# Optimization experiments

Hardware: AMD Instinct MI355X
Metric: run time of the kernel (lower is better)

Reference implementation:

```python
import jax, jax.numpy as jnp
import numpy as np

D_MODEL = 768; D_STATE = 64; D_CONV = 7; EXPAND = 2; HEADDIM = 64; NGROUPS = 1; CHUNK = 256
D_INNER = EXPAND * D_MODEL                                      # 1536
NHEADS = D_INNER // HEADDIM                                     # 24
D_IN_PROJ = 2 * D_INNER + 2 * NGROUPS * D_STATE + 2 * NHEADS    # 3248
CONV_DIM = D_INNER + 2 * NGROUPS * D_STATE                      # 1664
BATCH, SEQLEN = 2, 4096
EPS = 1e-5


def setup_inputs() -> dict:
    key = jax.random.key(0)
    ks = jax.random.split(key, 8)
    w = lambda k, shape, s=0.02: jax.random.normal(k, shape, jnp.float32) * s
    # dt in [1e-3, 1e-1], dt_bias = softplus^{-1}(dt)
    dt0 = jnp.exp(jax.random.uniform(ks[3], (NHEADS,)) * (np.log(0.1) - np.log(0.001)) + np.log(0.001))
    return {
        "x": jax.random.normal(ks[0], (BATCH, SEQLEN, D_MODEL), jnp.float32),
        "ln_w": jnp.ones((D_MODEL,), jnp.float32),
        "ln_b": jnp.zeros((D_MODEL,), jnp.float32),
        "in_proj_w": w(ks[1], (D_IN_PROJ, D_MODEL)),
        "conv_w": w(ks[2], (CONV_DIM, D_CONV), 0.2),
        "conv_b": jnp.zeros((CONV_DIM,), jnp.float32),
        "dt_bias": dt0 + jnp.log(-jnp.expm1(-dt0)),
        "A_log": jnp.log(jax.random.uniform(ks[4], (NHEADS,), minval=1.0, maxval=16.0)),
        "D": jnp.ones((NHEADS,), jnp.float32),
        "fc_D_w": w(ks[5], (NHEADS, D_INNER)),
        "rms_w": jnp.ones((D_INNER,), jnp.float32),
        "out_proj_w": w(ks[6], (D_MODEL, D_INNER)),
    }


def _segsum(a):
    # a: (..., T) -> (..., T, T) lower-triangular segment sums, -inf above diagonal
    T = a.shape[-1]
    cs = jnp.cumsum(a, -1)
    ss = cs[..., :, None] - cs[..., None, :]
    return jnp.where(jnp.tril(jnp.ones((T, T), bool)), ss, -jnp.inf)


def _ssd(X, A, Bm, Cm):
    # Chunked SSD scan (mamba_chunk_scan_combined, D=None, z=None, ngroups=1).
    # X: (b,l,h,p) already scaled by dt; A: (b,l,h) = dt*A_head; Bm,Cm: (b,l,n)
    b, l, h, p = X.shape
    c = l // CHUNK
    X = X.reshape(b, c, CHUNK, h, p)
    A = A.reshape(b, c, CHUNK, h).transpose(0, 3, 1, 2)  # (b,h,c,l)
    Bm = Bm.reshape(b, c, CHUNK, D_STATE)
    Cm = Cm.reshape(b, c, CHUNK, D_STATE)
    A_cum = jnp.cumsum(A, -1)
    Lmat = jnp.exp(_segsum(A))                                      # (b,h,c,l,s)
    Y_diag = jnp.einsum("bcln,bcsn,bhcls,bcshp->bclhp", Cm, Bm, Lmat, X)
    decay_states = jnp.exp(A_cum[..., -1:] - A_cum)                 # (b,h,c,l)
    states = jnp.einsum("bcln,bhcl,bclhp->bchpn", Bm, decay_states, X)
    A_chunk = jnp.pad(A_cum[..., -1], ((0, 0), (0, 0), (1, 0)))     # (b,h,c+1)
    decay_chunk = jnp.exp(_segsum(A_chunk))                         # (b,h,c+1,c+1)
    all_states = jnp.concatenate([jnp.zeros_like(states[:, :1]), states], 1)
    prev = jnp.einsum("bhzc,bchpn->bzhpn", decay_chunk, all_states)[:, :-1]
    Y_off = jnp.einsum("bcln,bchpn,bhcl->bclhp", Cm, prev, jnp.exp(A_cum))
    return (Y_diag + Y_off).reshape(b, l, h, p)


def _dwconv_causal(x, w, b):
    # x: (B,L,C), w: (C,K); torch Conv1d(padding=K-1) then [:, :L] == causal conv
    xp = jnp.pad(x, ((0, 0), (D_CONV - 1, 0), (0, 0))).transpose(0, 2, 1)
    y = jax.lax.conv_general_dilated(xp, w[:, None, :], (1,), "VALID",
                                     feature_group_count=CONV_DIM,
                                     dimension_numbers=("NCH", "OIH", "NCH"))
    return y.transpose(0, 2, 1) + b


def _forward(x, ln_w, ln_b, in_proj_w, conv_w, conv_b, dt_bias, A_log, D, fc_D_w, rms_w, out_proj_w):
    B, L, _ = x.shape
    # pre-LayerNorm
    mu = jnp.mean(x, -1, keepdims=True)
    var = jnp.mean((x - mu) ** 2, -1, keepdims=True)
    u = (x - mu) * jax.lax.rsqrt(var + EPS) * ln_w + ln_b
    # input projection -> z | xBC | dt_fw,dt_bw
    zxbcdt = u @ in_proj_w.T
    z = zxbcdt[..., :D_INNER]
    xBC = zxbcdt[..., D_INNER:D_INNER + CONV_DIM]
    dt2 = zxbcdt[..., -2 * NHEADS:]
    dt = jnp.concatenate([dt2[..., :NHEADS], jnp.flip(dt2[..., NHEADS:], 1)], 0)  # (2B,L,H)
    dt = jax.nn.softplus(dt + dt_bias)
    A = -jnp.exp(A_log)
    # causal depthwise conv + SiLU
    xBC = jax.nn.silu(_dwconv_causal(xBC, conv_w, conv_b))
    xs = xBC[..., :D_INNER]
    Bm = xBC[..., D_INNER:D_INNER + D_STATE]
    Cm = xBC[..., D_INNER + D_STATE:]
    x_og = xs
    cat2 = lambda t: jnp.concatenate([t, jnp.flip(t, 1)], 0)  # fwd + reversed copy
    X = cat2(xs).reshape(2 * B, L, NHEADS, HEADDIM) * dt[..., None]
    y = _ssd(X, dt * A, cat2(Bm), cat2(Cm)).reshape(2 * B, L, D_INNER)
    # quasiseparable combine: shift each direction by one, zero the boundary
    y = jnp.roll(y, 1, axis=1).at[:, 0, :].set(0.0)
    y = y[:B] + jnp.flip(y[B:], 1)
    # data-dependent diagonal term
    Dterm = x_og @ fc_D_w.T + D                                 # (B,L,H)
    y = y + x_og * jnp.repeat(Dterm, HEADDIM, axis=-1)
    # gated RMSNorm
    y = y * jax.nn.silu(z)
    y = y * jax.lax.rsqrt(jnp.mean(y * y, -1, keepdims=True) + EPS) * rms_w
    # out projection + residual (dropout=0 -> identity)
    return y @ out_proj_w.T + x


def reference(x, ln_w, ln_b, in_proj_w, conv_w, conv_b, dt_bias, A_log, D, fc_D_w, rms_w, out_proj_w):
    return _forward(x, ln_w, ln_b, in_proj_w, conv_w, conv_b, dt_bias, A_log, D, fc_D_w, rms_w, out_proj_w)
```

## Files before the change

### kernel.cpp

```cpp
#include <hip/hip_runtime.h>
#include <hip/hip_bf16.h>
#include <cstdint>
#include <cstddef>

typedef __hip_bfloat16 bf16;
typedef __attribute__((ext_vector_type(8))) short short8;
typedef __attribute__((ext_vector_type(4))) float f32x4;

#define B_   2
#define L_   4096
#define DM_  768
#define DI_  1536
#define NH_  24
#define HD_  64
#define DS_  64
#define CH_  256
#define NC_  16
#define CD_  1664
#define DIP_ 3248
#define EPS_ 1e-5f

#define ROWS_ (B_*L_)
#define BB4_  (2*B_)

#define LDSK 40
#define LDT  72

__device__ __forceinline__ float b2f(bf16 v) { return __bfloat162float(v); }
__device__ __forceinline__ bf16  f2b(float v) { return __float2bfloat16(v); }
__device__ __forceinline__ float sb2f(short s) {
    bf16 t; __builtin_memcpy(&t, &s, 2); return __bfloat162float(t);
}
__device__ __forceinline__ short f2s(float v) {
    bf16 t = __float2bfloat16(v); short s; __builtin_memcpy(&s, &t, 2); return s;
}

__global__ __launch_bounds__(256) void cast_f2b(const float* __restrict__ s,
                                                bf16* __restrict__ d, int n) {
    int i = (blockIdx.x * 256 + threadIdx.x) * 4;
    if (i + 3 < n) {
        float4 v = *(const float4*)(s + i);
        d[i]   = f2b(v.x); d[i+1] = f2b(v.y);
        d[i+2] = f2b(v.z); d[i+3] = f2b(v.w);
    } else {
        for (int k = i; k < n; k++) d[k] = f2b(s[k]);
    }
}

__global__ __launch_bounds__(256) void ln_kernel(const float* __restrict__ x,
                                                 const float* __restrict__ w,
                                                 const float* __restrict__ bb,
                                                 bf16* __restrict__ u) {
    int row = blockIdx.x, tid = threadIdx.x;
    const float* xr = x + (size_t)row * DM_;
    float v0 = xr[tid], v1 = xr[tid + 256], v2 = xr[tid + 512];
    float s = v0 + v1 + v2;
    float q = v0*v0 + v1*v1 + v2*v2;
    for (int off = 32; off > 0; off >>= 1) {
        s += __shfl_down(s, off);
        q += __shfl_down(q, off);
    }
    __shared__ float rs[4], rq[4];
    __shared__ float mean_s, rstd_s;
    int lane = tid & 63, wid = tid >> 6;
    if (!lane) { rs[wid] = s; rq[wid] = q; }
    __syncthreads();
    if (!tid) {
        float S = rs[0]+rs[1]+rs[2]+rs[3];
        float Q = rq[0]+rq[1]+rq[2]+rq[3];
        float mu = S / (float)DM_;
        float var = Q / (float)DM_ - mu*mu;
        mean_s = mu; rstd_s = rsqrtf(var + EPS_);
    }
    __syncthreads();
    float mu = mean_s, rstd = rstd_s;
    bf16* ur = u + (size_t)row * DM_;
    ur[tid]       = f2b((v0 - mu) * rstd * w[tid]       + bb[tid]);
    ur[tid + 256] = f2b((v1 - mu) * rstd * w[tid + 256] + bb[tid + 256]);
    ur[tid + 512] = f2b((v2 - mu) * rstd * w[tid + 512] + bb[tid + 512]);
}

__global__ __launch_bounds__(256) void gemm_bf16_inproj(const bf16* __restrict__ A,
                                                        const bf16* __restrict__ W,
                                                        bf16* __restrict__ zbuf,
                                                        bf16* __restrict__ xbc,
                                                        float* __restrict__ dtr) {
    __shared__ short As[128 * LDSK];
    __shared__ short Ws[128 * LDSK];
    int tid = threadIdx.x;
    int wave = tid >> 6, lane = tid & 63;
    int wm = (wave >> 1) * 64, wn = (wave & 1) * 64;
    int bm = blockIdx.y * 128, bn = blockIdx.x * 128;
    f32x4 acc[4][4] = {};
    int lr = tid >> 1;
    int lseg = (tid & 1) * 16;
    const int K = DM_;
    int fr = lane & 15, kg = (lane >> 4) * 8;
    for (int k0 = 0; k0 < K; k0 += 32) {
        const short* ag = (const short*)A + (size_t)(bm + lr) * K + k0 + lseg;
        short8 av0 = *(const short8*)ag;
        short8 av1 = *(const short8*)(ag + 8);
        short8 wv0 = {}, wv1 = {};
        int n = bn + lr;
        if (n < DIP_) {
            const short* wg = (const short*)W + (size_t)n * K + k0 + lseg;
            wv0 = *(const short8*)wg;
            wv1 = *(const short8*)(wg + 8);
        }
        __syncthreads();
        *(short8*)&As[lr*LDSK + lseg]     = av0;
        *(short8*)&As[lr*LDSK + lseg + 8] = av1;
        *(short8*)&Ws[lr*LDSK + lseg]     = wv0;
        *(short8*)&Ws[lr*LDSK + lseg + 8] = wv1;
        __syncthreads();
        short8 af[4], wf[4];
        #pragma unroll
        for (int i = 0; i < 4; i++)
            af[i] = *(const short8*)&As[(wm + i*16 + fr)*LDSK + kg];
        #pragma unroll
        for (int j = 0; j < 4; j++)
            wf[j] = *(const short8*)&Ws[(wn + j*16 + fr)*LDSK + kg];
        #pragma unroll
        for (int i = 0; i < 4; i++)
            #pragma unroll
            for (int j = 0; j < 4; j++)
                acc[i][j] = __builtin_amdgcn_mfma_f32_16x16x32_bf16(af[i], wf[j], acc[i][j], 0, 0, 0);
    }
    int rg = (lane >> 4) * 4;
    #pragma unroll
    for (int i = 0; i < 4; i++) {
        int mrow = bm + wm + i*16 + rg;
        #pragma unroll
        for (int j = 0; j < 4; j++) {
            int ncol = bn + wn + j*16 + fr;
            #pragma unroll
            for (int r = 0; r < 4; r++) {
                float v = acc[i][j][r];
                int m = mrow + r;
                if (ncol < DI_)            zbuf[(size_t)m * DI_ + ncol] = f2b(v);
                else if (ncol < DI_ + CD_) xbc[(size_t)m * CD_ + (ncol - DI_)] = f2b(v);
                else if (ncol < DIP_)      dtr[(size_t)m * 48 + (ncol - DI_ - CD_)] = v;
            }
        }
    }
}

__global__ __launch_bounds__(256) void gemm_bf16_out(const bf16* __restrict__ A,
                                                     const bf16* __restrict__ W,
                                                     const float* __restrict__ resid,
                                                     float* __restrict__ C) {
    __shared__ short As[128 * LDSK];
    __shared__ short Ws[128 * LDSK];
    int tid = threadIdx.x;
    int wave = tid >> 6, lane = tid & 63;
    int wm = (wave >> 1) * 64, wn = (wave & 1) * 64;
    int bm = blockIdx.y * 128, bn = blockIdx.x * 128;
    f32x4 acc[4][4] = {};
    int lr = tid >> 1;
    int lseg = (tid & 1) * 16;
    const int K = DI_;
    int fr = lane & 15, kg = (lane >> 4) * 8;
    for (int k0 = 0; k0 < K; k0 += 32) {
        const short* ag = (const short*)A + (size_t)(bm + lr) * K + k0 + lseg;
        short8 av0 = *(const short8*)ag;
        short8 av1 = *(const short8*)(ag + 8);
        const short* wg = (const short*)W + (size_t)(bn + lr) * K + k0 + lseg;
        short8 wv0 = *(const short8*)wg;
        short8 wv1 = *(const short8*)(wg + 8);
        __syncthreads();
        *(short8*)&As[lr*LDSK + lseg]     = av0;
        *(short8*)&As[lr*LDSK + lseg + 8] = av1;
        *(short8*)&Ws[lr*LDSK + lseg]     = wv0;
        *(short8*)&Ws[lr*LDSK + lseg + 8] = wv1;
        __syncthreads();
        short8 af[4], wf[4];
        #pragma unroll
        for (int i = 0; i < 4; i++)
            af[i] = *(const short8*)&As[(wm + i*16 + fr)*LDSK + kg];
        #pragma unroll
        for (int j = 0; j < 4; j++)
            wf[j] = *(const short8*)&Ws[(wn + j*16 + fr)*LDSK + kg];
        #pragma unroll
        for (int i = 0; i < 4; i++)
            #pragma unroll
            for (int j = 0; j < 4; j++)
                acc[i][j] = __builtin_amdgcn_mfma_f32_16x16x32_bf16(af[i], wf[j], acc[i][j], 0, 0, 0);
    }
    int rg = (lane >> 4) * 4;
    #pragma unroll
    for (int i = 0; i < 4; i++) {
        int mrow = bm + wm + i*16 + rg;
        #pragma unroll
        for (int j = 0; j < 4; j++) {
            int ncol = bn + wn + j*16 + fr;
            #pragma unroll
            for (int r = 0; r < 4; r++) {
                int m = mrow + r;
                C[(size_t)m * DM_ + ncol] = acc[i][j][r] + resid[(size_t)m * DM_ + ncol];
            }
        }
    }
}

__global__ __launch_bounds__(256) void conv_kernel(const bf16* __restrict__ xbc,
                                                   const float* __restrict__ cw,
                                                   const float* __restrict__ cb,
                                                   bf16* __restrict__ out) {
    size_t idx = (size_t)blockIdx.x * 256 + threadIdx.x;
    if (idx >= (size_t)ROWS_ * CD_) return;
    int c = idx % CD_;
    int t = (idx / CD_) % L_;
    int b = idx / ((size_t)CD_ * L_);
    float acc = cb[c];
    #pragma unroll
    for (int j = 0; j < 7; j++) {
        int tt = t - 6 + j;
        if (tt >= 0)
            acc += b2f(xbc[((size_t)(b * L_ + tt)) * CD_ + c]) * cw[c * 7 + j];
    }
    acc = acc / (1.f + __expf(-acc));
    out[idx] = f2b(acc);
}

__global__ __launch_bounds__(256) void dt_kernel(const float* __restrict__ dtr,
                                                 const float* __restrict__ dt_bias,
                                                 float* __restrict__ dt4) {
    int idx = blockIdx.x * 256 + threadIdx.x;
    if (idx >= BB4_ * L_ * NH_) return;
    int h = idx % NH_;
    int t = (idx / NH_) % L_;
    int bbx = idx / (NH_ * L_);
    int bp = bbx & 1;
    float raw;
    if (bbx < 2) raw = dtr[((size_t)(bp * L_ + t)) * 48 + h];
    else         raw = dtr[((size_t)(bp * L_ + (L_ - 1 - t))) * 48 + NH_ + h];
    float v = raw + dt_bias[h];
    float dt = (v > 20.f) ? v : log1pf(__expf(v));
    dt4[idx] = dt;
}

__global__ __launch_bounds__(256) void scan_kernel(const float* __restrict__ dt4,
                                                   const float* __restrict__ A_log,
                                                   float* __restrict__ Acum) {
    int bid = blockIdx.x;
    int c  = bid % NC_;
    int h  = (bid / NC_) % NH_;
    int bbx = bid / (NC_ * NH_);
    int l = threadIdx.x;
    float Ah = -__expf(A_log[h]);
    float val = dt4[((size_t)(bbx * L_) + c * CH_ + l) * NH_ + h] * Ah;
    __shared__ float sc[256];
    sc[l] = val; __syncthreads();
    for (int off = 1; off < 256; off <<= 1) {
        float t = (l >= off) ? sc[l - off] : 0.f;
        __syncthreads();
        sc[l] += t;
        __syncthreads();
    }
    Acum[(size_t)bid * CH_ + l] = sc[l];
}

__global__ __launch_bounds__(256) void states_kernel(const bf16* __restrict__ conv,
                                                     const float* __restrict__ dt4,
                                                     const float* __restrict__ Acum,
                                                     bf16* __restrict__ states) {
    int bid = blockIdx.x;
    int h = bid % NH_;
    int c = (bid / NH_) % NC_;
    int bbx = bid / (NH_ * NC_);
    int bp = bbx & 1;
    bool flip = bbx >= 2;
    int tid = threadIdx.x;
    int wave = tid >> 6, lane = tid & 63;
    int wr = wave >> 1, wc = wave & 1;
    int fr = lane & 15, kg = (lane >> 4) * 8, rg = (lane >> 4) * 4;
    size_t abase = ((size_t)(bbx * NH_ + h) * NC_ + c) * CH_;
    float Atot = Acum[abase + CH_ - 1];

    __shared__ short Xt[64 * LDT];
    __shared__ short Bdt[64 * LDT];
    f32x4 acc[2][2] = {};

    for (int lt = 0; lt < 4; lt++) {
        __syncthreads();
        int l = tid & 63;
        int q0 = (tid >> 6) * 8;
        int t = c * CH_ + lt * 64 + l;
        int tt = flip ? (L_ - 1 - t) : t;
        const short* crow = (const short*)conv + (size_t)(bp * L_ + tt) * CD_;
        float dtv = dt4[((size_t)(bbx * L_) + t) * NH_ + h];
        float decay = __expf(Atot - Acum[abase + lt * 64 + l]);
        #pragma unroll
        for (int half = 0; half < 2; half++) {
            int qq = q0 + half * 32;
            short8 xv = *(const short8*)(crow + h * HD_ + qq);
            short8 bv = *(const short8*)(crow + DI_ + qq);
            #pragma unroll
            for (int k = 0; k < 8; k++) {
                Xt[(qq + k) * LDT + l]  = f2s(sb2f(xv[k]) * dtv);
                Bdt[(qq + k) * LDT + l] = f2s(sb2f(bv[k]) * decay);
            }
        }
        __syncthreads();
        #pragma unroll
        for (int ks = 0; ks < 2; ks++) {
            short8 af[2], wf[2];
            #pragma unroll
            for (int i = 0; i < 2; i++)
                af[i] = *(const short8*)&Xt[(wr*32 + i*16 + fr)*LDT + ks*32 + kg];
            #pragma unroll
            for (int j = 0; j < 2; j++)
                wf[j] = *(const short8*)&Bdt[(wc*32 + j*16 + fr)*LDT + ks*32 + kg];
            #pragma unroll
            for (int i = 0; i < 2; i++)
                #pragma unroll
                for (int j = 0; j < 2; j++)
                    acc[i][j] = __builtin_amdgcn_mfma_f32_16x16x32_bf16(af[i], wf[j], acc[i][j], 0, 0, 0);
        }
    }
    size_t sbase = (size_t)bid * 4096;
    #pragma unroll
    for (int i = 0; i < 2; i++)
        #pragma unroll
        for (int j = 0; j < 2; j++)
            #pragma unroll
            for (int r = 0; r < 4; r++) {
                int p = wr*32 + i*16 + rg + r;
                int n = wc*32 + j*16 + fr;
                states[sbase + p*64 + n] = f2b(acc[i][j][r]);
            }
}

__global__ __launch_bounds__(256) void chunkscan_kernel(const bf16* __restrict__ states,
                                                        const float* __restrict__ Acum,
                                                        bf16* __restrict__ prev) {
    int bid = blockIdx.x;
    int h = bid % NH_;
    int bbx = bid / NH_;
    int tid = threadIdx.x;
    float run[16];
    #pragma unroll
    for (int k = 0; k < 16; k++) run[k] = 0.f;
    for (int c = 0; c < NC_; c++) {
        float Tc = Acum[((size_t)(bbx * NH_ + h) * NC_ + c) * CH_ + CH_ - 1];
        float ec = __expf(Tc);
        size_t base = ((size_t)(bbx * NC_ + c) * NH_ + h) * 4096;
        #pragma unroll
        for (int k = 0; k < 16; k++) {
            size_t e = tid + k * 256;
            prev[base + e] = f2b(run[k]);
            run[k] = run[k] * ec + b2f(states[base + e]);
        }
    }
}

__global__ __launch_bounds__(256) void ydiag_kernel(const bf16* __restrict__ conv,
                                                    const float* __restrict__ dt4,
                                                    const float* __restrict__ Acum,
                                                    const bf16* __restrict__ prev,
                                                    bf16* __restrict__ yc,
                                                    int pass) {
    int bid = blockIdx.x;
    int lt = bid & 3;
    int q  = bid >> 2;
    int h  = q % NH_;
    int r2 = q / NH_;
    int c  = r2 % NC_;
    int b  = r2 / NC_;
    int bbx = pass ? (b + 2) : b;
    int bp = b;
    bool flip = pass != 0;
    int tid = threadIdx.x;
    int wave = tid >> 6, lane = tid & 63;
    int wr = wave >> 1, wc = wave & 1;
    int fr = lane & 15, kg = (lane >> 4) * 8, rg = (lane >> 4) * 4;
    size_t abase = ((size_t)(bbx * NH_ + h) * NC_ + c) * CH_;

    __shared__ short Ct[64 * LDT];
    __shared__ short Pt[64 * LDT];
    __shared__ short Xt[64 * LDT];
    __shared__ short Gt[64 * LDT];
    __shared__ float aL[64], aS[64];

    #pragma unroll
    for (int it = 0; it < 2; it++) {
        int li = tid + it * 256;
        int l = li >> 3, cs = (li & 7) * 8;
        int t = c * CH_ + lt * 64 + l;
        int tt = flip ? (L_ - 1 - t) : t;
        *(short8*)&Ct[l * LDT + cs] =
            *(const short8*)((const short*)conv + (size_t)(bp * L_ + tt) * CD_ + DI_ + DS_ + cs);
    }
    {
        size_t pbase = ((size_t)(bbx * NC_ + c) * NH_ + h) * 4096;
        #pragma unroll
        for (int it = 0; it < 2; it++) {
            int li = tid + it * 256;
            int p = li >> 3, cs = (li & 7) * 8;
            *(short8*)&Pt[p * LDT + cs] =
                *(const short8*)((const short*)prev + pbase + p * 64 + cs);
        }
    }
    if (tid < 64) aL[tid] = Acum[abase + lt * 64 + tid];
    __syncthreads();

    f32x4 acc[2][2] = {};
    #pragma unroll
    for (int ks = 0; ks < 2; ks++) {
        short8 af[2], wf[2];
        #pragma unroll
        for (int i = 0; i < 2; i++)
            af[i] = *(const short8*)&Ct[(wr*32 + i*16 + fr)*LDT + ks*32 + kg];
        #pragma unroll
        for (int j = 0; j < 2; j++)
            wf[j] = *(const short8*)&Pt[(wc*32 + j*16 + fr)*LDT + ks*32 + kg];
        #pragma unroll
        for (int i = 0; i < 2; i++)
            #pragma unroll
            for (int j = 0; j < 2; j++)
                acc[i][j] = __builtin_amdgcn_mfma_f32_16x16x32_bf16(af[i], wf[j], acc[i][j], 0, 0, 0);
    }
    #pragma unroll
    for (int i = 0; i < 2; i++)
        #pragma unroll
        for (int r = 0; r < 4; r++) {
            float e = __expf(aL[wr*32 + i*16 + rg + r]);
            #pragma unroll
            for (int j = 0; j < 2; j++) acc[i][j][r] *= e;
        }

    for (int st = 0; st <= lt; st++) {
        __syncthreads();
        #pragma unroll
        for (int it = 0; it < 2; it++) {
            int li = tid + it * 256;
            int s = li >> 3, cs = (li & 7) * 8;
            int t = c * CH_ + st * 64 + s;
            int tt = flip ? (L_ - 1 - t) : t;
            *(short8*)&Pt[s * LDT + cs] =
                *(const short8*)((const short*)conv + (size_t)(bp * L_ + tt) * CD_ + DI_ + cs);
        }
        {
            int s = tid & 63;
            int p0 = (tid >> 6) * 8;
            int t = c * CH_ + st * 64 + s;
            int tt = flip ? (L_ - 1 - t) : t;
            const short* crow = (const short*)conv + (size_t)(bp * L_ + tt) * CD_ + h * HD_;
            float dtv = dt4[((size_t)(bbx * L_) + t) * NH_ + h];
            #pragma unroll
            for (int half = 0; half < 2; half++) {
                int p = p0 + half * 32;
                short8 xv = *(const short8*)(crow + p);
                #pragma unroll
                for (int k = 0; k < 8; k++)
                    Xt[(p + k) * LDT + s] = f2s(sb2f(xv[k]) * dtv);
            }
        }
        if (tid < 64) aS[tid] = Acum[abase + st * 64 + tid];
        __syncthreads();
        f32x4 gacc[2][2] = {};
        #pragma unroll
        for (int ks = 0; ks < 2; ks++) {
            short8 af[2], wf[2];
            #pragma unroll
            for (int i = 0; i < 2; i++)
                af[i] = *(const short8*)&Ct[(wr*32 + i*16 + fr)*LDT + ks*32 + kg];
            #pragma unroll
            for (int j = 0; j < 2; j++)
                wf[j] = *(const short8*)&Pt[(wc*32 + j*16 + fr)*LDT + ks*32 + kg];
            #pragma unroll
            for (int i = 0; i < 2; i++)
                #pragma unroll
                for (int j = 0; j < 2; j++)
                    gacc[i][j] = __builtin_amdgcn_mfma_f32_16x16x32_bf16(af[i], wf[j], gacc[i][j], 0, 0, 0);
        }
        #pragma unroll
        for (int i = 0; i < 2; i++)
            #pragma unroll
            for (int j = 0; j < 2; j++)
                #pragma unroll
                for (int r = 0; r < 4; r++) {
                    int ll = wr*32 + i*16 + rg + r;
                    int ss = wc*32 + j*16 + fr;
                    bool valid = (st < lt) || (ll >= ss);
                    float g = valid ? gacc[i][j][r] * __expf(aL[ll] - aS[ss]) : 0.f;
                    Gt[ll * LDT + ss] = f2s(g);
                }
        __syncthreads();
        #pragma unroll
        for (int ks = 0; ks < 2; ks++) {
            short8 af[2], wf[2];
            #pragma unroll
            for (int i = 0; i < 2; i++)
                af[i] = *(const short8*)&Gt[(wr*32 + i*16 + fr)*LDT + ks*32 + kg];
            #pragma unroll
            for (int j = 0; j < 2; j++)
                wf[j] = *(const short8*)&Xt[(wc*32 + j*16 + fr)*LDT + ks*32 + kg];
            #pragma unroll
            for (int i = 0; i < 2; i++)
                #pragma unroll
                for (int j = 0; j < 2; j++)
                    acc[i][j] = __builtin_amdgcn_mfma_f32_16x16x32_bf16(af[i], wf[j], acc[i][j], 0, 0, 0);
        }
    }

    #pragma unroll
    for (int i = 0; i < 2; i++)
        #pragma unroll
        for (int r = 0; r < 4; r++) {
            int l = wr*32 + i*16 + rg + r;
            int t = c * CH_ + lt * 64 + l;
            #pragma unroll
            for (int j = 0; j < 2; j++) {
                int p = wc*32 + j*16 + fr;
                float v = acc[i][j][r];
                if (!pass) {
                    int pos = t + 1;
                    if (pos == L_)
                        yc[((size_t)(b * L_)) * DI_ + h * HD_ + p] = f2b(0.f);
                    else
                        yc[((size_t)(b * L_) + pos) * DI_ + h * HD_ + p] = f2b(v);
                } else {
                    int pos = L_ - 2 - t;
                    if (pos >= 0) {
                        size_t o = ((size_t)(b * L_) + pos) * DI_ + h * HD_ + p;
                        yc[o] = f2b(b2f(yc[o]) + v);
                    }
                }
            }
        }
}

__global__ __launch_bounds__(256) void combine_kernel(const bf16* __restrict__ yc,
                                                      const bf16* __restrict__ conv,
                                                      const bf16* __restrict__ zbuf,
                                                      const float* __restrict__ fcD,
                                                      const float* __restrict__ Dvec,
                                                      const float* __restrict__ rms_w,
                                                      bf16* __restrict__ ybuf) {
    int row = blockIdx.x;
    int tid = threadIdx.x;
    __shared__ float xog_s[DI_];
    __shared__ float dterm_s[NH_];
    __shared__ float rs[4];
    __shared__ float scale_s;
    float yv[6], xog[6], zv[6];
    const bf16* convrow = conv + (size_t)row * CD_;
    const bf16* zrow = zbuf + (size_t)row * DI_;
    const bf16* ycrow = yc + (size_t)row * DI_;
    #pragma unroll
    for (int k = 0; k < 6; k++) {
        int d = tid + k * 256;
        float xo = b2f(convrow[d]);
        xog[k] = xo; xog_s[d] = xo;
        zv[k] = b2f(zrow[d]);
        yv[k] = b2f(ycrow[d]);
    }
    __syncthreads();
    int wid = tid >> 6, lane = tid & 63;
    for (int hh = 0; hh < 6; hh++) {
        int h = wid * 6 + hh;
        float s = 0.f;
        #pragma unroll
        for (int k = 0; k < 24; k++) {
            int d = lane + k * 64;
            s += xog_s[d] * fcD[(size_t)h * DI_ + d];
        }
        for (int off = 32; off > 0; off >>= 1) s += __shfl_down(s, off);
        if (!lane) dterm_s[h] = s + Dvec[h];
    }
    __syncthreads();
    float ss = 0.f;
    #pragma unroll
    for (int k = 0; k < 6; k++) {
        int d = tid + k * 256;
        int h = d >> 6;
        float y = yv[k] + xog[k] * dterm_s[h];
        float z = zv[k];
        y *= z / (1.f + __expf(-z));
        yv[k] = y;
        ss += y * y;
    }
    for (int off = 32; off > 0; off >>= 1) ss += __shfl_down(ss, off);
    if (!lane) rs[wid] = ss;
    __syncthreads();
    if (!tid) scale_s = rsqrtf((rs[0]+rs[1]+rs[2]+rs[3]) / (float)DI_ + EPS_);
    __syncthreads();
    float sc = scale_s;
    bf16* yrow = ybuf + (size_t)row * DI_;
    #pragma unroll
    for (int k = 0; k < 6; k++) {
        int d = tid + k * 256;
        yrow[d] = f2b(yv[k] * sc * rms_w[d]);
    }
}

extern "C" void kernel_launch(void* const* d_in, const int* in_sizes, int n_in,
                              void* d_out, int out_size, void* d_ws, size_t ws_size,
                              hipStream_t stream) {
    const float* x        = (const float*)d_in[0];
    const float* ln_w     = (const float*)d_in[1];
    const float* ln_b     = (const float*)d_in[2];
    const float* in_proj  = (const float*)d_in[3];
    const float* conv_w   = (const float*)d_in[4];
    const float* conv_b   = (const float*)d_in[5];
    const float* dt_bias  = (const float*)d_in[6];
    const float* A_log    = (const float*)d_in[7];
    const float* Dvec     = (const float*)d_in[8];
    const float* fc_D_w   = (const float*)d_in[9];
    const float* rms_w    = (const float*)d_in[10];
    const float* out_proj = (const float*)d_in[11];
    float* out = (float*)d_out;

    uint8_t* base = (uint8_t*)d_ws;
    size_t off = 0;
    auto alloc = [&](size_t bytes) -> void* {
        void* p = base + off;
        off += (bytes + 255) & ~(size_t)255;
        return p;
    };
    bf16*  buf_z    = (bf16*) alloc((size_t)ROWS_ * DI_ * 2);
    uint8_t* regA   = (uint8_t*)alloc((size_t)ROWS_ * CD_ * 2);
    float* buf_dtr  = (float*)alloc((size_t)ROWS_ * 48 * 4);
    bf16*  buf_conv = (bf16*) alloc((size_t)ROWS_ * CD_ * 2);
    float* buf_dt   = (float*)alloc((size_t)BB4_ * L_ * NH_ * 4);
    float* buf_acum = (float*)alloc((size_t)BB4_ * NH_ * NC_ * CH_ * 4);
    uint8_t* regB   = (uint8_t*)alloc((size_t)ROWS_ * DM_ * 4);
    bf16*  w_in_bf  = (bf16*) alloc((size_t)DIP_ * DM_ * 2);
    bf16*  w_out_bf = (bf16*) alloc((size_t)DM_ * DI_ * 2);

    bf16*  buf_xbc  = (bf16*)regA;
    bf16*  buf_st   = (bf16*)regA;
    bf16*  buf_prev = buf_st + (size_t)BB4_ * NC_ * NH_ * 4096;
    bf16*  buf_y    = (bf16*)regA;
    bf16*  buf_u    = (bf16*)regB;
    bf16*  buf_yc   = (bf16*)regB;

    cast_f2b<<<(DIP_ * DM_ / 4 + 255) / 256, 256, 0, stream>>>(in_proj, w_in_bf, DIP_ * DM_);
    cast_f2b<<<(DM_ * DI_ / 4 + 255) / 256, 256, 0, stream>>>(out_proj, w_out_bf, DM_ * DI_);
    ln_kernel<<<ROWS_, 256, 0, stream>>>(x, ln_w, ln_b, buf_u);
    gemm_bf16_inproj<<<dim3((DIP_ + 127) / 128, ROWS_ / 128), 256, 0, stream>>>(
        buf_u, w_in_bf, buf_z, buf_xbc, buf_dtr);
    {
        size_t tot = (size_t)ROWS_ * CD_;
        conv_kernel<<<(tot + 255) / 256, 256, 0, stream>>>(buf_xbc, conv_w, conv_b, buf_conv);
    }
    dt_kernel<<<(BB4_ * L_ * NH_) / 256, 256, 0, stream>>>(buf_dtr, dt_bias, buf_dt);
    scan_kernel<<<BB4_ * NH_ * NC_, 256, 0, stream>>>(buf_dt, A_log, buf_acum);
    states_kernel<<<BB4_ * NC_ * NH_, 256, 0, stream>>>(buf_conv, buf_dt, buf_acum, buf_st);
    chunkscan_kernel<<<BB4_ * NH_, 256, 0, stream>>>(buf_st, buf_acum, buf_prev);
    ydiag_kernel<<<B_ * NC_ * NH_ * 4, 256, 0, stream>>>(buf_conv, buf_dt, buf_acum, buf_prev, buf_yc, 0);
    ydiag_kernel<<<B_ * NC_ * NH_ * 4, 256, 0, stream>>>(buf_conv, buf_dt, buf_acum, buf_prev, buf_yc, 1);
    combine_kernel<<<ROWS_, 256, 0, stream>>>(buf_yc, buf_conv, buf_z, fc_D_w, Dvec, rms_w, buf_y);
    gemm_bf16_out<<<dim3(DM_ / 128, ROWS_ / 128), 256, 0, stream>>>(
        buf_y, w_out_bf, x, out);
}
```

Measured before the change: 547.6 us.

## Pretranspose dt-scaled X and B, vectorize conv, load MFMA operands from global

Adds an xt_kernel that writes dt-scaled X and raw B once into time-contiguous transposed buffers. The states and ydiag kernels then read their MFMA fragments directly from global memory instead of rebuilding LDS tiles with scalar transposes in every block and every inner step. The depthwise conv is rewritten so each thread handles 8 channels by 4 timesteps with vector loads and reused weights, and chunkscan now works in place on a single states buffer. The cost is an extra kernel, two new workspace buffers and more global traffic for the transposed copies.

```diff
diff --git a/kernel.cpp b/kernel.cpp
--- a/kernel.cpp
+++ b/kernel.cpp
@@ -206,20 +206,55 @@
                                                    const float* __restrict__ cw,
                                                    const float* __restrict__ cb,
                                                    bf16* __restrict__ out) {
-    size_t idx = (size_t)blockIdx.x * 256 + threadIdx.x;
-    if (idx >= (size_t)ROWS_ * CD_) return;
-    int c = idx % CD_;
-    int t = (idx / CD_) % L_;
-    int b = idx / ((size_t)CD_ * L_);
-    float acc = cb[c];
-    #pragma unroll
-    for (int j = 0; j < 7; j++) {
-        int tt = t - 6 + j;
-        if (tt >= 0)
-            acc += b2f(xbc[((size_t)(b * L_ + tt)) * CD_ + c]) * cw[c * 7 + j];
-    }
-    acc = acc / (1.f + __expf(-acc));
-    out[idx] = f2b(acc);
+    int g = blockIdx.x * 256 + threadIdx.x;
+    int cg = g % 208;
+    int tq = g / 208;
+    int b = tq >> 10;
+    int t0 = (tq & 1023) * 4;
+    int c8 = cg * 8;
+    const short* src = (const short*)xbc + (size_t)(b * L_) * CD_ + c8;
+
+    float w[7][8], acc[4][8];
+    #pragma unroll
+    for (int k = 0; k < 8; k++) {
+        #pragma unroll
+        for (int j = 0; j < 7; j++) w[j][k] = cw[(c8 + k) * 7 + j];
+        float bias = cb[c8 + k];
+        #pragma unroll
+        for (int q = 0; q < 4; q++) acc[q][k] = bias;
+    }
+    #pragma unroll
+    for (int m = 0; m < 10; m++) {
+        int tt = t0 - 6 + m;
+        float row[8];
+        if (tt >= 0) {
+            short8 v = *(const short8*)(src + (size_t)tt * CD_);
+            #pragma unroll
+            for (int k = 0; k < 8; k++) row[k] = sb2f(v[k]);
+        } else {
+            #pragma unroll
+            for (int k = 0; k < 8; k++) row[k] = 0.f;
+        }
+        #pragma unroll
+        for (int q = 0; q < 4; q++) {
+            int j = m - q;
+            if (j >= 0 && j < 7) {
+                #pragma unroll
+                for (int k = 0; k < 8; k++) acc[q][k] += row[k] * w[j][k];
+            }
+        }
+    }
+    #pragma unroll
+    for (int q = 0; q < 4; q++) {
+        short8 o;
+        #pragma unroll
+        for (int k = 0; k < 8; k++) {
+            float a = acc[q][k];
+            a = a / (1.f + __expf(-a));
+            o[k] = f2s(a);
+        }
+        *(short8*)((short*)out + (size_t)(b * L_ + t0 + q) * CD_ + c8) = o;
+    }
 }
 
 __global__ __launch_bounds__(256) void dt_kernel(const float* __restrict__ dtr,
@@ -260,57 +295,91 @@
     Acum[(size_t)bid * CH_ + l] = sc[l];
 }
 
-__global__ __launch_bounds__(256) void states_kernel(const bf16* __restrict__ conv,
-                                                     const float* __restrict__ dt4,
+__global__ __launch_bounds__(256) void xt_kernel(const bf16* __restrict__ conv,
+                                                 const float* __restrict__ dt4,
+                                                 bf16* __restrict__ XT,
+                                                 bf16* __restrict__ BT) {
+    int bid = blockIdx.x;
+    int hh = bid % 25;
+    int c  = (bid / 25) % NC_;
+    int bbx = bid / (25 * NC_);
+    int bp = bbx & 1;
+    bool flip = bbx >= 2;
+    bool isB = (hh == NH_);
+    int coff = isB ? DI_ : hh * HD_;
+    int tid = threadIdx.x;
+    __shared__ short tile[64][72];
+    short* dstb = (short*)(isB ? BT : XT);
+    size_t rowbase = isB ? (size_t)(bbx * 64) : (size_t)((bbx * NH_ + hh) * 64);
+    for (int lt = 0; lt < 4; lt++) {
+        __syncthreads();
+        #pragma unroll
+        for (int it = 0; it < 2; it++) {
+            int li = tid + it * 256;
+            int r = li >> 3, seg = (li & 7) * 8;
+            int t = c * CH_ + lt * 64 + r;
+            int tt = flip ? (L_ - 1 - t) : t;
+            short8 v = *(const short8*)((const short*)conv + (size_t)(bp * L_ + tt) * CD_ + coff + seg);
+            if (!isB) {
+                float dtv = dt4[((size_t)(bbx * L_) + t) * NH_ + hh];
+                #pragma unroll
+                for (int k = 0; k < 8; k++) v[k] = f2s(sb2f(v[k]) * dtv);
+            }
+            *(short8*)&tile[r][seg] = v;
+        }
+        __syncthreads();
+        #pragma unroll
+        for (int it = 0; it < 2; it++) {
+            int li = tid + it * 256;
+            int p = li >> 3, seg = (li & 7) * 8;
+            short8 o;
+            #pragma unroll
+            for (int k = 0; k < 8; k++) o[k] = tile[seg + k][p];
+            *(short8*)(dstb + (rowbase + p) * L_ + c * CH_ + lt * 64 + seg) = o;
+        }
+    }
+}
+
+__global__ __launch_bounds__(256) void states_kernel(const bf16* __restrict__ XT,
+                                                     const bf16* __restrict__ BT,
                                                      const float* __restrict__ Acum,
                                                      bf16* __restrict__ states) {
     int bid = blockIdx.x;
     int h = bid % NH_;
     int c = (bid / NH_) % NC_;
     int bbx = bid / (NH_ * NC_);
-    int bp = bbx & 1;
-    bool flip = bbx >= 2;
     int tid = threadIdx.x;
     int wave = tid >> 6, lane = tid & 63;
     int wr = wave >> 1, wc = wave & 1;
     int fr = lane & 15, kg = (lane >> 4) * 8, rg = (lane >> 4) * 4;
     size_t abase = ((size_t)(bbx * NH_ + h) * NC_ + c) * CH_;
-    float Atot = Acum[abase + CH_ - 1];
-
-    __shared__ short Xt[64 * LDT];
-    __shared__ short Bdt[64 * LDT];
+    __shared__ float dec[256];
+    {
+        float Atot = Acum[abase + CH_ - 1];
+        dec[tid] = __expf(Atot - Acum[abase + tid]);
+    }
+    __syncthreads();
+    const short* xbase = (const short*)XT + (size_t)((bbx * NH_ + h) * 64) * L_ + c * CH_;
+    const short* bbase = (const short*)BT + (size_t)(bbx * 64) * L_ + c * CH_;
     f32x4 acc[2][2] = {};
-
     for (int lt = 0; lt < 4; lt++) {
-        __syncthreads();
-        int l = tid & 63;
-        int q0 = (tid >> 6) * 8;
-        int t = c * CH_ + lt * 64 + l;
-        int tt = flip ? (L_ - 1 - t) : t;
-        const short* crow = (const short*)conv + (size_t)(bp * L_ + tt) * CD_;
-        float dtv = dt4[((size_t)(bbx * L_) + t) * NH_ + h];
-        float decay = __expf(Atot - Acum[abase + lt * 64 + l]);
-        #pragma unroll
-        for (int half = 0; half < 2; half++) {
-            int qq = q0 + half * 32;
-            short8 xv = *(const short8*)(crow + h * HD_ + qq);
-            short8 bv = *(const short8*)(crow + DI_ + qq);
-            #pragma unroll
-            for (int k = 0; k < 8; k++) {
-                Xt[(qq + k) * LDT + l]  = f2s(sb2f(xv[k]) * dtv);
-                Bdt[(qq + k) * LDT + l] = f2s(sb2f(bv[k]) * decay);
-            }
-        }
-        __syncthreads();
         #pragma unroll
         for (int ks = 0; ks < 2; ks++) {
+            int l0 = lt * 64 + ks * 32 + kg;
+            float d[8];
+            #pragma unroll
+            for (int k = 0; k < 8; k++) d[k] = dec[l0 + k];
             short8 af[2], wf[2];
             #pragma unroll
             for (int i = 0; i < 2; i++)
-                af[i] = *(const short8*)&Xt[(wr*32 + i*16 + fr)*LDT + ks*32 + kg];
-            #pragma unroll
-            for (int j = 0; j < 2; j++)
-                wf[j] = *(const short8*)&Bdt[(wc*32 + j*16 + fr)*LDT + ks*32 + kg];
+                af[i] = *(const short8*)(xbase + (size_t)(wr*32 + i*16 + fr) * L_ + l0);
+            #pragma unroll
+            for (int j = 0; j < 2; j++) {
+                short8 raw = *(const short8*)(bbase + (size_t)(wc*32 + j*16 + fr) * L_ + l0);
+                #pragma unroll
+                for (int k = 0; k < 8; k++) raw[k] = f2s(sb2f(raw[k]) * d[k]);
+                wf[j] = raw;
+            }
             #pragma unroll
             for (int i = 0; i < 2; i++)
                 #pragma unroll
@@ -331,9 +400,8 @@
             }
 }
 
-__global__ __launch_bounds__(256) void chunkscan_kernel(const bf16* __restrict__ states,
-                                                        const float* __restrict__ Acum,
-                                                        bf16* __restrict__ prev) {
+__global__ __launch_bounds__(256) void chunkscan_kernel(bf16* __restrict__ sp,
+                                                        const float* __restrict__ Acum) {
     int bid = blockIdx.x;
     int h = bid % NH_;
     int bbx = bid / NH_;
@@ -348,14 +416,15 @@
         #pragma unroll
         for (int k = 0; k < 16; k++) {
             size_t e = tid + k * 256;
-            prev[base + e] = f2b(run[k]);
-            run[k] = run[k] * ec + b2f(states[base + e]);
+            float sv = b2f(sp[base + e]);
+            sp[base + e] = f2b(run[k]);
+            run[k] = run[k] * ec + sv;
         }
     }
 }
 
 __global__ __launch_bounds__(256) void ydiag_kernel(const bf16* __restrict__ conv,
-                                                    const float* __restrict__ dt4,
+                                                    const bf16* __restrict__ XT,
                                                     const float* __restrict__ Acum,
                                                     const bf16* __restrict__ prev,
                                                     bf16* __restrict__ yc,
@@ -376,50 +445,35 @@
     int fr = lane & 15, kg = (lane >> 4) * 8, rg = (lane >> 4) * 4;
     size_t abase = ((size_t)(bbx * NH_ + h) * NC_ + c) * CH_;
 
-    __shared__ short Ct[64 * LDT];
-    __shared__ short Pt[64 * LDT];
-    __shared__ short Xt[64 * LDT];
     __shared__ short Gt[64 * LDT];
     __shared__ float aL[64], aS[64];
-
-    #pragma unroll
-    for (int it = 0; it < 2; it++) {
-        int li = tid + it * 256;
-        int l = li >> 3, cs = (li & 7) * 8;
+    if (tid < 64) aL[tid] = Acum[abase + lt * 64 + tid];
+
+    short8 cf[2][2];
+    #pragma unroll
+    for (int i = 0; i < 2; i++) {
+        int l = wr*32 + i*16 + fr;
         int t = c * CH_ + lt * 64 + l;
         int tt = flip ? (L_ - 1 - t) : t;
-        *(short8*)&Ct[l * LDT + cs] =
-            *(const short8*)((const short*)conv + (size_t)(bp * L_ + tt) * CD_ + DI_ + DS_ + cs);
-    }
-    {
-        size_t pbase = ((size_t)(bbx * NC_ + c) * NH_ + h) * 4096;
-        #pragma unroll
-        for (int it = 0; it < 2; it++) {
-            int li = tid + it * 256;
-            int p = li >> 3, cs = (li & 7) * 8;
-            *(short8*)&Pt[p * LDT + cs] =
-                *(const short8*)((const short*)prev + pbase + p * 64 + cs);
-        }
-    }
-    if (tid < 64) aL[tid] = Acum[abase + lt * 64 + tid];
-    __syncthreads();
+        const short* crow = (const short*)conv + (size_t)(bp * L_ + tt) * CD_ + DI_ + DS_;
+        #pragma unroll
+        for (int ks = 0; ks < 2; ks++)
+            cf[i][ks] = *(const short8*)(crow + ks*32 + kg);
+    }
 
     f32x4 acc[2][2] = {};
+    size_t pbase = ((size_t)(bbx * NC_ + c) * NH_ + h) * 4096;
     #pragma unroll
     for (int ks = 0; ks < 2; ks++) {
-        short8 af[2], wf[2];
-        #pragma unroll
-        for (int i = 0; i < 2; i++)
-            af[i] = *(const short8*)&Ct[(wr*32 + i*16 + fr)*LDT + ks*32 + kg];
-        #pragma unroll
-        for (int j = 0; j < 2; j++)
-            wf[j] = *(const short8*)&Pt[(wc*32 + j*16 + fr)*LDT + ks*32 + kg];
-        #pragma unroll
-        for (int i = 0; i < 2; i++)
-            #pragma unroll
-            for (int j = 0; j < 2; j++)
-                acc[i][j] = __builtin_amdgcn_mfma_f32_16x16x32_bf16(af[i], wf[j], acc[i][j], 0, 0, 0);
-    }
+        #pragma unroll
+        for (int j = 0; j < 2; j++) {
+            short8 pf = *(const short8*)((const short*)prev + pbase + (size_t)(wc*32 + j*16 + fr)*64 + ks*32 + kg);
+            #pragma unroll
+            for (int i = 0; i < 2; i++)
+                acc[i][j] = __builtin_amdgcn_mfma_f32_16x16x32_bf16(cf[i][ks], pf, acc[i][j], 0, 0, 0);
+        }
+    }
+    __syncthreads();
     #pragma unroll
     for (int i = 0; i < 2; i++)
         #pragma unroll
@@ -429,51 +483,26 @@
             for (int j = 0; j < 2; j++) acc[i][j][r] *= e;
         }
 
+    const short* xbase = (const short*)XT + (size_t)((bbx * NH_ + h) * 64) * L_ + c * CH_;
+
     for (int st = 0; st <= lt; st++) {
-        __syncthreads();
-        #pragma unroll
-        for (int it = 0; it < 2; it++) {
-            int li = tid + it * 256;
-            int s = li >> 3, cs = (li & 7) * 8;
+        if (tid < 64) aS[tid] = Acum[abase + st * 64 + tid];
+        f32x4 gacc[2][2] = {};
+        #pragma unroll
+        for (int j = 0; j < 2; j++) {
+            int s = wc*32 + j*16 + fr;
             int t = c * CH_ + st * 64 + s;
             int tt = flip ? (L_ - 1 - t) : t;
-            *(short8*)&Pt[s * LDT + cs] =
-                *(const short8*)((const short*)conv + (size_t)(bp * L_ + tt) * CD_ + DI_ + cs);
-        }
-        {
-            int s = tid & 63;
-            int p0 = (tid >> 6) * 8;
-            int t = c * CH_ + st * 64 + s;
-            int tt = flip ? (L_ - 1 - t) : t;
-            const short* crow = (const short*)conv + (size_t)(bp * L_ + tt) * CD_ + h * HD_;
-            float dtv = dt4[((size_t)(bbx * L_) + t) * NH_ + h];
-            #pragma unroll
-            for (int half = 0; half < 2; half++) {
-                int p = p0 + half * 32;
-                short8 xv = *(const short8*)(crow + p);
+            const short* brow = (const short*)conv + (size_t)(bp * L_ + tt) * CD_ + DI_;
+            #pragma unroll
+            for (int ks = 0; ks < 2; ks++) {
+                short8 bf = *(const short8*)(brow + ks*32 + kg);
                 #pragma unroll
-                for (int k = 0; k < 8; k++)
-                    Xt[(p + k) * LDT + s] = f2s(sb2f(xv[k]) * dtv);
-            }
-        }
-        if (tid < 64) aS[tid] = Acum[abase + st * 64 + tid];
-        __syncthreads();
-        f32x4 gacc[2][2] = {};
-        #pragma unroll
-        for (int ks = 0; ks < 2; ks++) {
-            short8 af[2], wf[2];
-            #pragma unroll
-            for (int i = 0; i < 2; i++)
-                af[i] = *(const short8*)&Ct[(wr*32 + i*16 + fr)*LDT + ks*32 + kg];
-            #pragma unroll
-            for (int j = 0; j < 2; j++)
-                wf[j] = *(const short8*)&Pt[(wc*32 + j*16 + fr)*LDT + ks*32 + kg];
-            #pragma unroll
-            for (int i = 0; i < 2; i++)
-                #pragma unroll
-                for (int j = 0; j < 2; j++)
-                    gacc[i][j] = __builtin_amdgcn_mfma_f32_16x16x32_bf16(af[i], wf[j], gacc[i][j], 0, 0, 0);
-        }
+                for (int i = 0; i < 2; i++)
+                    gacc[i][j] = __builtin_amdgcn_mfma_f32_16x16x32_bf16(cf[i][ks], bf, gacc[i][j], 0, 0, 0);
+            }
+        }
+        __syncthreads();
         #pragma unroll
         for (int i = 0; i < 2; i++)
             #pragma unroll
@@ -489,19 +518,20 @@
         __syncthreads();
         #pragma unroll
         for (int ks = 0; ks < 2; ks++) {
-            short8 af[2], wf[2];
+            short8 gf[2], xf[2];
             #pragma unroll
             for (int i = 0; i < 2; i++)
-                af[i] = *(const short8*)&Gt[(wr*32 + i*16 + fr)*LDT + ks*32 + kg];
+                gf[i] = *(const short8*)&Gt[(wr*32 + i*16 + fr)*LDT + ks*32 + kg];
             #pragma unroll
             for (int j = 0; j < 2; j++)
-                wf[j] = *(const short8*)&Xt[(wc*32 + j*16 + fr)*LDT + ks*32 + kg];
+                xf[j] = *(const short8*)(xbase + (size_t)(wc*32 + j*16 + fr)*L_ + st*64 + ks*32 + kg);
             #pragma unroll
             for (int i = 0; i < 2; i++)
                 #pragma unroll
                 for (int j = 0; j < 2; j++)
-                    acc[i][j] = __builtin_amdgcn_mfma_f32_16x16x32_bf16(af[i], wf[j], acc[i][j], 0, 0, 0);
-        }
+                    acc[i][j] = __builtin_amdgcn_mfma_f32_16x16x32_bf16(gf[i], xf[j], acc[i][j], 0, 0, 0);
+        }
+        __syncthreads();
     }
 
     #pragma unroll
@@ -628,10 +658,11 @@
     uint8_t* regB   = (uint8_t*)alloc((size_t)ROWS_ * DM_ * 4);
     bf16*  w_in_bf  = (bf16*) alloc((size_t)DIP_ * DM_ * 2);
     bf16*  w_out_bf = (bf16*) alloc((size_t)DM_ * DI_ * 2);
+    bf16*  buf_XT   = (bf16*) alloc((size_t)BB4_ * NH_ * 64 * L_ * 2);
+    bf16*  buf_BT   = (bf16*) alloc((size_t)BB4_ * 64 * L_ * 2);
 
     bf16*  buf_xbc  = (bf16*)regA;
-    bf16*  buf_st   = (bf16*)regA;
-    bf16*  buf_prev = buf_st + (size_t)BB4_ * NC_ * NH_ * 4096;
+    bf16*  buf_sp   = (bf16*)regA;
     bf16*  buf_y    = (bf16*)regA;
     bf16*  buf_u    = (bf16*)regB;
     bf16*  buf_yc   = (bf16*)regB;
@@ -641,16 +672,14 @@
     ln_kernel<<<ROWS_, 256, 0, stream>>>(x, ln_w, ln_b, buf_u);
     gemm_bf16_inproj<<<dim3((DIP_ + 127) / 128, ROWS_ / 128), 256, 0, stream>>>(
         buf_u, w_in_bf, buf_z, buf_xbc, buf_dtr);
-    {
-        size_t tot = (size_t)ROWS_ * CD_;
-        conv_kernel<<<(tot + 255) / 256, 256, 0, stream>>>(buf_xbc, conv_w, conv_b, buf_conv);
-    }
+    conv_kernel<<<(ROWS_ / 4) * (CD_ / 8) / 256, 256, 0, stream>>>(buf_xbc, conv_w, conv_b, buf_conv);
     dt_kernel<<<(BB4_ * L_ * NH_) / 256, 256, 0, stream>>>(buf_dtr, dt_bias, buf_dt);
     scan_kernel<<<BB4_ * NH_ * NC_, 256, 0, stream>>>(buf_dt, A_log, buf_acum);
-    states_kernel<<<BB4_ * NC_ * NH_, 256, 0, stream>>>(buf_conv, buf_dt, buf_acum, buf_st);
-    chunkscan_kernel<<<BB4_ * NH_, 256, 0, stream>>>(buf_st, buf_acum, buf_prev);
-    ydiag_kernel<<<B_ * NC_ * NH_ * 4, 256, 0, stream>>>(buf_conv, buf_dt, buf_acum, buf_prev, buf_yc, 0);
-    ydiag_kernel<<<B_ * NC_ * NH_ * 4, 256, 0, stream>>>(buf_conv, buf_dt, buf_acum, buf_prev, buf_yc, 1);
+    xt_kernel<<<BB4_ * NC_ * 25, 256, 0, stream>>>(buf_conv, buf_dt, buf_XT, buf_BT);
+    states_kernel<<<BB4_ * NC_ * NH_, 256, 0, stream>>>(buf_XT, buf_BT, buf_acum, buf_sp);
+    chunkscan_kernel<<<BB4_ * NH_, 256, 0, stream>>>(buf_sp, buf_acum);
+    ydiag_kernel<<<B_ * NC_ * NH_ * 4, 256, 0, stream>>>(buf_conv, buf_XT, buf_acum, buf_sp, buf_yc, 0);
+    ydiag_kernel<<<B_ * NC_ * NH_ * 4, 256, 0, stream>>>(buf_conv, buf_XT, buf_acum, buf_sp, buf_yc, 1);
     combine_kernel<<<ROWS_, 256, 0, stream>>>(buf_yc, buf_conv, buf_z, fc_D_w, Dvec, rms_w, buf_y);
     gemm_bf16_out<<<dim3(DM_ / 128, ROWS_ / 128), 256, 0, stream>>>(
         buf_y, w_out_bf, x, out);
```

After: 532.6 us. 2.7% less time.
